# Kernel tuning notes

Measured on AMD Instinct MI355X. Metric: run time of the kernel, lower is better.

The kernel has to match this reference:

```python
import jax, jax.numpy as jnp
import numpy as np

B, S, H, L = 64, 512, 1024, 9  # batch, seq_len, hidden_size, num_labels


def setup_inputs() -> dict:
    key = jax.random.key(0)
    ks = jax.random.split(key, 8)
    hidden = jax.random.normal(ks[0], (B, S, H), dtype=jnp.float32)
    W = jax.random.normal(ks[1], (L, H), dtype=jnp.float32) * 0.02
    b = jnp.zeros((L,), dtype=jnp.float32)
    # pytorch-crf initializes transitions uniform in [-0.1, 0.1]
    start_transitions = jax.random.uniform(ks[2], (L,), jnp.float32, -0.1, 0.1)
    end_transitions = jax.random.uniform(ks[3], (L,), jnp.float32, -0.1, 0.1)
    transitions = jax.random.uniform(ks[4], (L, L), jnp.float32, -0.1, 0.1)
    labels = jax.random.randint(ks[5], (B, S), 0, L)
    # variable lengths; first timestep always valid (required by pytorch-crf)
    lengths = jax.random.randint(ks[6], (B,), S // 4, S + 1)
    mask = (jnp.arange(S)[None, :] < lengths[:, None]).astype(jnp.int32)
    return {
        "hidden": hidden, "W": W, "b": b,
        "start_transitions": start_transitions,
        "end_transitions": end_transitions,
        "transitions": transitions,
        "labels": labels, "mask": mask,
    }


def reference(hidden, W, b, start_transitions, end_transitions, transitions, labels, mask):
    # classifier: emissions [B,S,L] (fp32, matching .float() cast in the module)
    emissions = jnp.einsum("bsh,lh->bsl", hidden, W) + b
    maskf = mask.astype(emissions.dtype)

    # ---- numerator: score of the gold path ----
    emit = jnp.take_along_axis(emissions, labels[..., None], axis=-1)[..., 0]  # [B,S]
    trans_sc = transitions[labels[:, :-1], labels[:, 1:]]                       # [B,S-1]
    score = (start_transitions[labels[:, 0]]
             + jnp.sum(emit * maskf, axis=1)
             + jnp.sum(trans_sc * maskf[:, 1:], axis=1))
    seq_ends = jnp.sum(mask, axis=1) - 1                     # last valid index per example
    last_tags = labels[jnp.arange(labels.shape[0]), seq_ends]
    score = score + end_transitions[last_tags]

    # ---- denominator: log partition via masked forward recurrence ----
    alpha0 = start_transitions[None, :] + emissions[:, 0]    # [B,L]
    em_t = jnp.swapaxes(emissions, 0, 1)[1:]                 # [S-1,B,L]
    mk_t = jnp.swapaxes(mask, 0, 1)[1:].astype(bool)         # [S-1,B]

    def step(alpha, xs):
        e_t, m_t = xs
        # broadcast: alpha[b,i] + transitions[i,j] + e_t[b,j]
        nxt = jax.scipy.special.logsumexp(
            alpha[:, :, None] + transitions[None, :, :] + e_t[:, None, :], axis=1)
        alpha = jnp.where(m_t[:, None], nxt, alpha)
        return alpha, None

    alpha, _ = jax.lax.scan(step, alpha0, (em_t, mk_t))
    logZ = jax.scipy.special.logsumexp(alpha + end_transitions[None, :], axis=1)  # [B]

    llh = score - logZ
    loss = -jnp.mean(llh)  # reduction='mean', negated in the module
    return loss
```

## Files before the change

### kernel.cpp

```cpp
#include <hip/hip_runtime.h>
#include <hip/hip_bf16.h>

#define LOG2E 1.4426950408889634f
#define LN2   0.6931471805599453f

constexpr int Bn = 64, Sn = 512, Hn = 1024, Ln = 9;
constexpr int CL = 24;
constexpr int NC = 22;

typedef __attribute__((ext_vector_type(8))) short short8v;
typedef __attribute__((ext_vector_type(4))) float f32x4;

__device__ __forceinline__ float fexp2(float x) {
    float r; asm("v_exp_f32 %0, %1" : "=v"(r) : "v"(x)); return r;
}
__device__ __forceinline__ float flog2(float x) {
    float r; asm("v_log_f32 %0, %1" : "=v"(r) : "v"(x)); return r;
}
__device__ __forceinline__ unsigned cvtpk(float lo, float hi) {
    unsigned r; asm("v_cvt_pk_bf16_f32 %0, %1, %2" : "=v"(r) : "v"(lo), "v"(hi)); return r;
}
__device__ __forceinline__ float max9(const float* s) {
    return fmaxf(fmaxf(fmaxf(s[0], s[1]), fmaxf(s[2], s[3])),
                 fmaxf(fmaxf(s[4], s[5]), fmaxf(s[6], fmaxf(s[7], s[8]))));
}

__global__ __launch_bounds__(256) void emis_kernel(
    const float* __restrict__ hidden, const float* __restrict__ W,
    const float* __restrict__ bias, float* __restrict__ emis,
    float* __restrict__ out0)
{
    const int tid = threadIdx.x, lane = tid & 63, w = tid >> 6;

    if (blockIdx.x == 0 && tid == 0) out0[0] = 0.f;

    const int row0 = blockIdx.x * 64 + w * 16;
    const int col  = lane & 15;
    const int k0   = (lane >> 4) << 3;
    const float* hptr = hidden + (size_t)(row0 + col) * Hn + k0;
    const float* wptr = W + (size_t)(col < Ln ? col : Ln - 1) * Hn + k0;

    f32x4 acc = {0.f, 0.f, 0.f, 0.f};
    #pragma unroll 4
    for (int s = 0; s < 32; ++s) {
        f32x4 a0 = *(const f32x4*)(hptr + s * 32);
        f32x4 a1 = *(const f32x4*)(hptr + s * 32 + 4);
        f32x4 b0 = *(const f32x4*)(wptr + s * 32);
        f32x4 b1 = *(const f32x4*)(wptr + s * 32 + 4);
        uint4 ap, bp;
        ap.x = cvtpk(a0[0], a0[1]); ap.y = cvtpk(a0[2], a0[3]);
        ap.z = cvtpk(a1[0], a1[1]); ap.w = cvtpk(a1[2], a1[3]);
        bp.x = cvtpk(b0[0], b0[1]); bp.y = cvtpk(b0[2], b0[3]);
        bp.z = cvtpk(b1[0], b1[1]); bp.w = cvtpk(b1[2], b1[3]);
        short8v Av = *(short8v*)&ap;
        short8v Bv = *(short8v*)&bp;
        acc = __builtin_amdgcn_mfma_f32_16x16x32_bf16(Av, Bv, acc, 0, 0, 0);
    }

    if (col < Ln) {
        const float bv = bias[col];
        #pragma unroll
        for (int r = 0; r < 4; ++r) {
            const int row = ((lane >> 4) << 2) + r;
            emis[(size_t)(row0 + row) * Ln + col] = acc[r] + bv;
        }
    }
}

__global__ __launch_bounds__(256, 1) void crf_kernel(
    const float* __restrict__ emis, const float* __restrict__ st,
    const float* __restrict__ et,   const float* __restrict__ T,
    const int* __restrict__ labels, const int* __restrict__ mask,
    float* __restrict__ out)
{
    __shared__ __align__(16) float e_lds[Sn * Ln];
    __shared__ float M_lds[NC][Ln][10];
    __shared__ float part[4];
    __shared__ int   sl_sh;

    const int b    = blockIdx.x;
    const int tid  = threadIdx.x;
    const int w    = tid >> 6;
    const int lane = tid & 63;

    {
        const float4* src = (const float4*)(emis + (size_t)b * Sn * Ln);
        float4* dst = (float4*)e_lds;
        for (int i = tid; i < (Sn * Ln) / 4; i += 256) dst[i] = src[i];
    }
    float E[Ln][Ln];
    #pragma unroll
    for (int k = 0; k < Ln; ++k)
        #pragma unroll
        for (int j = 0; j < Ln; ++j)
            E[k][j] = fexp2(T[k * Ln + j] * LOG2E);
    if (w == 3) {
        const int* mb = mask + b * Sn;
        int s = 0;
        #pragma unroll
        for (int r = 0; r < Sn / 64; ++r) s += mb[lane + r * 64];
        #pragma unroll
        for (int off = 32; off; off >>= 1) s += __shfl_xor(s, off);
        if (lane == 0) sl_sh = s;
    }
    __syncthreads();

    const int sl    = sl_sh;
    const int nreal = (sl - 1 + CL - 1) / CL;

    {
        const int ul = lane / 9;
        const int i  = lane - ul * 9;
        const int c  = w * 7 + ul;
        const int t0 = 1 + c * CL;
        if (ul < 7 && c < nreal) {
            const int nst = min(CL, sl - t0);
            float u[Ln];
            {
                const float* e0 = e_lds + t0 * Ln;
                #pragma unroll
                for (int j = 0; j < Ln; ++j)
                    u[j] = E[i][j] * fexp2(fmaf(e0[j], LOG2E, -4.f));
            }
            float extra = 0.f;
            for (int s = 1; s < nst; ++s) {
                const float* es = e_lds + (t0 + s) * Ln;
                float e2[Ln];
                #pragma unroll
                for (int j = 0; j < Ln; ++j) e2[j] = es[j];
                float v[Ln];
                #pragma unroll
                for (int j = 0; j < Ln; ++j) v[j] = 0.f;
                #pragma unroll
                for (int kk = 0; kk < Ln; ++kk) {
                    const float uk = u[kk];
                    #pragma unroll
                    for (int j = 0; j < Ln; ++j)
                        v[j] = fmaf(uk, E[kk][j], v[j]);
                }
                #pragma unroll
                for (int j = 0; j < Ln; ++j)
                    u[j] = v[j] * fexp2(fmaf(e2[j], LOG2E, -4.f));
                if (s == 12) {
                    float m  = max9(u);
                    float iv = 1.f / m;
                    #pragma unroll
                    for (int j = 0; j < Ln; ++j) u[j] *= iv;
                    extra = flog2(m);
                }
            }
            #pragma unroll
            for (int j = 0; j < Ln; ++j)
                M_lds[c][i][j] = flog2(u[j]) + extra + 4.f * (float)nst;
        }
    }
    __syncthreads();

    float logZ = 0.f;
    if (w == 0) {
        const int j9 = lane < Ln ? lane : Ln - 1;
        float al[Ln];
        #pragma unroll
        for (int j = 0; j < Ln; ++j) al[j] = (st[j] + e_lds[j]) * LOG2E;
        for (int c = 0; c < nreal; ++c) {
            float s[Ln];
            #pragma unroll
            for (int k = 0; k < Ln; ++k) s[k] = al[k] + M_lds[c][k][j9];
            float p = max9(s);
            float sum = fexp2(s[0] - p);
            #pragma unroll
            for (int k = 1; k < Ln; ++k) sum += fexp2(s[k] - p);
            float aj = p + flog2(sum);
            #pragma unroll
            for (int k = 0; k < Ln; ++k) al[k] = __shfl(aj, k);
        }
        float z[Ln];
        #pragma unroll
        for (int j = 0; j < Ln; ++j) z[j] = al[j] + et[j] * LOG2E;
        float p = max9(z);
        float sum = fexp2(z[0] - p);
        #pragma unroll
        for (int j = 1; j < Ln; ++j) sum += fexp2(z[j] - p);
        logZ = (p + flog2(sum)) * LN2;
    } else {
        const int* lb = labels + b * Sn;
        float sc = 0.f;
        for (int t = (w - 1) * 64 + lane; t < sl; t += 192) {
            int lt = lb[t];
            sc += e_lds[t * Ln + lt];
            if (t >= 1) sc += T[lb[t - 1] * Ln + lt];
        }
        #pragma unroll
        for (int off = 32; off; off >>= 1) sc += __shfl_xor(sc, off);
        if (w == 1 && lane == 0) sc += st[lb[0]] + et[lb[sl - 1]];
        if (lane == 0) part[w - 1] = sc;
    }
    __syncthreads();

    if (w == 0 && lane == 0) {
        float llh = part[0] + part[1] + part[2] - logZ;
        atomicAdd(out, llh * (-1.f / 64.f));
    }
}

extern "C" void kernel_launch(void* const* d_in, const int* in_sizes, int n_in,
                              void* d_out, int out_size, void* d_ws, size_t ws_size,
                              hipStream_t stream) {
    const float* hidden = (const float*)d_in[0];
    const float* W      = (const float*)d_in[1];
    const float* bias   = (const float*)d_in[2];
    const float* st     = (const float*)d_in[3];
    const float* et     = (const float*)d_in[4];
    const float* T      = (const float*)d_in[5];
    const int*   labels = (const int*)d_in[6];
    const int*   mask   = (const int*)d_in[7];

    float* emis = (float*)d_ws;
    float* outp = (float*)d_out;

    emis_kernel<<<512, 256, 0, stream>>>(hidden, W, bias, emis, outp);
    crf_kernel<<<Bn, 256, 0, stream>>>(emis, st, et, T, labels, mask, outp);
}
```

Before: 45.25 us.

## Fuse emission GEMM and CRF into one kernel with last-block reduction

Merges the emission projection and the CRF forward pass into a single kernel. Each block computes 64 timesteps of emissions into shared memory, then immediately builds 16-step chunk transfer matrices spread across 32 chunks per sequence. The last block of each batch row, found with an atomic counter, runs the serial chunk combination and the gold-path score. This removes the second launch and the round trip of the full emission tensor through global memory, and adds more parallel chunks. In exchange it needs two memsets, threadfence/atomic synchronisation, and a longer serial combine over up to 32 chunks.

After: 125.6 us. +177.6%, slower.

```diff
diff --git a/kernel.cpp b/kernel.cpp
--- a/kernel.cpp
+++ b/kernel.cpp
@@ -5,8 +5,6 @@
 #define LN2   0.6931471805599453f
 
 constexpr int Bn = 64, Sn = 512, Hn = 1024, Ln = 9;
-constexpr int CL = 24;
-constexpr int NC = 22;
 
 typedef __attribute__((ext_vector_type(8))) short short8v;
 typedef __attribute__((ext_vector_type(4))) float f32x4;
@@ -25,20 +23,26 @@
                  fmaxf(fmaxf(s[4], s[5]), fmaxf(s[6], fmaxf(s[7], s[8]))));
 }
 
-__global__ __launch_bounds__(256) void emis_kernel(
+__global__ __launch_bounds__(256, 2) void fused_kernel(
     const float* __restrict__ hidden, const float* __restrict__ W,
-    const float* __restrict__ bias, float* __restrict__ emis,
-    float* __restrict__ out0)
+    const float* __restrict__ bias,   const float* __restrict__ st,
+    const float* __restrict__ et,     const float* __restrict__ T,
+    const int* __restrict__ labels,   const int* __restrict__ mask,
+    float* __restrict__ Mbuf, float* __restrict__ eL, float* __restrict__ e0g,
+    int* __restrict__ done,   float* __restrict__ out)
 {
+    __shared__ __align__(16) float e_s[64][12];
+    __shared__ float M_lds[32 * 81];
+    __shared__ float part_s[4];
+    __shared__ int   sl_sh, last_sh;
+
     const int tid = threadIdx.x, lane = tid & 63, w = tid >> 6;
-
-    if (blockIdx.x == 0 && tid == 0) out0[0] = 0.f;
-
-    const int row0 = blockIdx.x * 64 + w * 16;
-    const int col  = lane & 15;
-    const int k0   = (lane >> 4) << 3;
-    const float* hptr = hidden + (size_t)(row0 + col) * Hn + k0;
-    const float* wptr = W + (size_t)(col < Ln ? col : Ln - 1) * Hn + k0;
+    const int bid = blockIdx.x, b = bid >> 3, rb = bid & 7;
+
+    const int col = lane & 15, g16 = lane >> 4;
+    const int row0 = b * Sn + rb * 64 + w * 16;
+    const float* hptr = hidden + (size_t)(row0 + col) * Hn + (g16 << 3);
+    const float* wptr = W + (size_t)(col < Ln ? col : Ln - 1) * Hn + (g16 << 3);
 
     f32x4 acc = {0.f, 0.f, 0.f, 0.f};
     #pragma unroll 4
@@ -61,73 +65,52 @@
         const float bv = bias[col];
         #pragma unroll
         for (int r = 0; r < 4; ++r) {
-            const int row = ((lane >> 4) << 2) + r;
-            emis[(size_t)(row0 + row) * Ln + col] = acc[r] + bv;
-        }
-    }
-}
-
-__global__ __launch_bounds__(256, 1) void crf_kernel(
-    const float* __restrict__ emis, const float* __restrict__ st,
-    const float* __restrict__ et,   const float* __restrict__ T,
-    const int* __restrict__ labels, const int* __restrict__ mask,
-    float* __restrict__ out)
-{
-    __shared__ __align__(16) float e_lds[Sn * Ln];
-    __shared__ float M_lds[NC][Ln][10];
-    __shared__ float part[4];
-    __shared__ int   sl_sh;
-
-    const int b    = blockIdx.x;
-    const int tid  = threadIdx.x;
-    const int w    = tid >> 6;
-    const int lane = tid & 63;
-
-    {
-        const float4* src = (const float4*)(emis + (size_t)b * Sn * Ln);
-        float4* dst = (float4*)e_lds;
-        for (int i = tid; i < (Sn * Ln) / 4; i += 256) dst[i] = src[i];
-    }
-    float E[Ln][Ln];
-    #pragma unroll
-    for (int k = 0; k < Ln; ++k)
-        #pragma unroll
-        for (int j = 0; j < Ln; ++j)
-            E[k][j] = fexp2(T[k * Ln + j] * LOG2E);
+            const int tl = w * 16 + (g16 << 2) + r;
+            const float v = acc[r] + bv;
+            e_s[tl][col] = v;
+            const int t = rb * 64 + tl;
+            if (col == labels[b * Sn + t]) eL[b * Sn + t] = v;
+        }
+    }
     if (w == 3) {
         const int* mb = mask + b * Sn;
         int s = 0;
         #pragma unroll
-        for (int r = 0; r < Sn / 64; ++r) s += mb[lane + r * 64];
+        for (int r = 0; r < 8; ++r) s += mb[lane + r * 64];
         #pragma unroll
         for (int off = 32; off; off >>= 1) s += __shfl_xor(s, off);
         if (lane == 0) sl_sh = s;
     }
     __syncthreads();
-
-    const int sl    = sl_sh;
-    const int nreal = (sl - 1 + CL - 1) / CL;
+    const int sl = sl_sh;
+
+    if (rb == 0 && tid < Ln) e0g[b * Ln + tid] = e_s[0][tid];
 
     {
-        const int ul = lane / 9;
-        const int i  = lane - ul * 9;
-        const int c  = w * 7 + ul;
-        const int t0 = 1 + c * CL;
-        if (ul < 7 && c < nreal) {
-            const int nst = min(CL, sl - t0);
+        const int c  = (rb << 2) + w;
+        const int g0 = max(16 * c, 1);
+        const int g1 = min(16 * c + 16, sl);
+        if (lane < Ln && g1 > g0) {
+            float E[Ln][Ln];
+            #pragma unroll
+            for (int k = 0; k < Ln; ++k)
+                #pragma unroll
+                for (int j = 0; j < Ln; ++j)
+                    E[k][j] = fexp2(T[k * Ln + j] * LOG2E);
+            const int i = lane, l0 = g0 - (rb << 6), nst = g1 - g0;
             float u[Ln];
             {
-                const float* e0 = e_lds + t0 * Ln;
+                const float* ep = e_s[l0];
                 #pragma unroll
                 for (int j = 0; j < Ln; ++j)
-                    u[j] = E[i][j] * fexp2(fmaf(e0[j], LOG2E, -4.f));
+                    u[j] = E[i][j] * fexp2(fmaf(ep[j], LOG2E, -4.f));
             }
             float extra = 0.f;
             for (int s = 1; s < nst; ++s) {
-                const float* es = e_lds + (t0 + s) * Ln;
-                float e2[Ln];
-                #pragma unroll
-                for (int j = 0; j < Ln; ++j) e2[j] = es[j];
+                const float* ep = e_s[l0 + s];
+                float q[Ln];
+                #pragma unroll
+                for (int j = 0; j < Ln; ++j) q[j] = fexp2(fmaf(ep[j], LOG2E, -4.f));
                 float v[Ln];
                 #pragma unroll
                 for (int j = 0; j < Ln; ++j) v[j] = 0.f;
@@ -135,37 +118,47 @@
                 for (int kk = 0; kk < Ln; ++kk) {
                     const float uk = u[kk];
                     #pragma unroll
-                    for (int j = 0; j < Ln; ++j)
-                        v[j] = fmaf(uk, E[kk][j], v[j]);
+                    for (int j = 0; j < Ln; ++j) v[j] = fmaf(uk, E[kk][j], v[j]);
                 }
                 #pragma unroll
-                for (int j = 0; j < Ln; ++j)
-                    u[j] = v[j] * fexp2(fmaf(e2[j], LOG2E, -4.f));
-                if (s == 12) {
-                    float m  = max9(u);
-                    float iv = 1.f / m;
+                for (int j = 0; j < Ln; ++j) u[j] = v[j] * q[j];
+                if (s == 8) {
+                    float m = max9(u), iv = 1.f / m;
                     #pragma unroll
                     for (int j = 0; j < Ln; ++j) u[j] *= iv;
                     extra = flog2(m);
                 }
             }
+            float* o = Mbuf + ((size_t)(b * 32 + c)) * 81 + i * Ln;
             #pragma unroll
             for (int j = 0; j < Ln; ++j)
-                M_lds[c][i][j] = flog2(u[j]) + extra + 4.f * (float)nst;
-        }
-    }
-    __syncthreads();
-
-    float logZ = 0.f;
+                o[j] = flog2(u[j]) + extra + 4.f * (float)nst;
+        }
+    }
+
+    __threadfence();
+    if (tid == 0) last_sh = (atomicAdd(&done[b], 1) == 7);
+    __syncthreads();
+    if (!last_sh) return;
+    __threadfence();
+
+    {
+        const float* src = Mbuf + (size_t)b * 32 * 81;
+        for (int i2 = tid; i2 < 32 * 81; i2 += 256) M_lds[i2] = src[i2];
+    }
+    __syncthreads();
+
     if (w == 0) {
         const int j9 = lane < Ln ? lane : Ln - 1;
         float al[Ln];
         #pragma unroll
-        for (int j = 0; j < Ln; ++j) al[j] = (st[j] + e_lds[j]) * LOG2E;
-        for (int c = 0; c < nreal; ++c) {
+        for (int j = 0; j < Ln; ++j) al[j] = (st[j] + e0g[b * Ln + j]) * LOG2E;
+        const int ncb = ((sl - 1) >> 4) + 1;
+        for (int c = 0; c < ncb; ++c) {
+            const float* mc = &M_lds[c * 81];
             float s[Ln];
             #pragma unroll
-            for (int k = 0; k < Ln; ++k) s[k] = al[k] + M_lds[c][k][j9];
+            for (int k = 0; k < Ln; ++k) s[k] = al[k] + mc[k * Ln + j9];
             float p = max9(s);
             float sum = fexp2(s[0] - p);
             #pragma unroll
@@ -181,24 +174,23 @@
         float sum = fexp2(z[0] - p);
         #pragma unroll
         for (int j = 1; j < Ln; ++j) sum += fexp2(z[j] - p);
-        logZ = (p + flog2(sum)) * LN2;
+        if (lane == 0) part_s[3] = (p + flog2(sum)) * LN2;
     } else {
         const int* lb = labels + b * Sn;
         float sc = 0.f;
         for (int t = (w - 1) * 64 + lane; t < sl; t += 192) {
-            int lt = lb[t];
-            sc += e_lds[t * Ln + lt];
-            if (t >= 1) sc += T[lb[t - 1] * Ln + lt];
+            sc += eL[b * Sn + t];
+            if (t >= 1) sc += T[lb[t - 1] * Ln + lb[t]];
         }
         #pragma unroll
         for (int off = 32; off; off >>= 1) sc += __shfl_xor(sc, off);
         if (w == 1 && lane == 0) sc += st[lb[0]] + et[lb[sl - 1]];
-        if (lane == 0) part[w - 1] = sc;
-    }
-    __syncthreads();
-
-    if (w == 0 && lane == 0) {
-        float llh = part[0] + part[1] + part[2] - logZ;
+        if (lane == 0) part_s[w - 1] = sc;
+    }
+    __syncthreads();
+
+    if (tid == 0) {
+        float llh = part_s[0] + part_s[1] + part_s[2] - part_s[3];
         atomicAdd(out, llh * (-1.f / 64.f));
     }
 }
@@ -215,9 +207,15 @@
     const int*   labels = (const int*)d_in[6];
     const int*   mask   = (const int*)d_in[7];
 
-    float* emis = (float*)d_ws;
+    float* Mbuf = (float*)d_ws;
+    float* eLp  = Mbuf + (size_t)Bn * 32 * 81;
+    float* e0g  = eLp + (size_t)Bn * Sn;
+    int*   done = (int*)(e0g + Bn * Ln);
     float* outp = (float*)d_out;
 
-    emis_kernel<<<512, 256, 0, stream>>>(hidden, W, bias, emis, outp);
-    crf_kernel<<<Bn, 256, 0, stream>>>(emis, st, et, T, labels, mask, outp);
-}
+    hipMemsetAsync(done, 0, Bn * sizeof(int), stream);
+    hipMemsetAsync(outp, 0, sizeof(float), stream);
+    fused_kernel<<<Bn * 8, 256, 0, stream>>>(hidden, W, bias, st, et, T,
+                                             labels, mask, Mbuf, eLp, e0g,
+                                             done, outp);
+}
```
